# Optimization experiments

Measured on AMD Instinct MI355X. Metric: run time of the kernel, lower is better.

The kernel has to match this reference:

```python
import jax, jax.numpy as jnp
import numpy as np

EMBED_DIM = 1024
N_HEADS = 16
HEAD_DIM = EMBED_DIM // N_HEADS


def setup_inputs() -> dict:
    key = jax.random.key(0)
    k_x, k_wqkv, k_bqkv, k_wo, k_bo = jax.random.split(key, 5)
    s = 1.0 / np.sqrt(EMBED_DIM)
    return {
        "x": jax.random.normal(k_x, (2, 2048, EMBED_DIM), dtype=jnp.float32),
        "w_qkv": jax.random.uniform(k_wqkv, (EMBED_DIM, 3 * EMBED_DIM), jnp.float32, -s, s),
        "b_qkv": jax.random.uniform(k_bqkv, (3 * EMBED_DIM,), jnp.float32, -s, s),
        "w_out": jax.random.uniform(k_wo, (EMBED_DIM, EMBED_DIM), jnp.float32, -s, s),
        "b_out": jax.random.uniform(k_bo, (EMBED_DIM,), jnp.float32, -s, s),
    }


def reference(x, w_qkv, b_qkv, w_out, b_out):
    B, T, C = x.shape
    qkv = x @ w_qkv + b_qkv                      # [B,T,3C]
    q, k, v = jnp.split(qkv, 3, axis=-1)
    # [B,T,C] -> [B,H,T,D]
    def heads(t):
        return t.reshape(B, T, N_HEADS, HEAD_DIM).transpose(0, 2, 1, 3)
    q, k, v = heads(q), heads(k), heads(v)
    scale = 1.0 / np.sqrt(HEAD_DIM).astype(np.float32)
    scores = jnp.einsum("bhqd,bhkd->bhqk", q, k) * scale
    causal = jnp.tril(jnp.ones((T, T), dtype=bool))  # True where allowed
    scores = jnp.where(causal, scores, jnp.finfo(scores.dtype).min)
    attn = jax.nn.softmax(scores, axis=-1)
    out = jnp.einsum("bhqk,bhkd->bhqd", attn, v)
    out = out.transpose(0, 2, 1, 3).reshape(B, T, C)
    return out @ w_out + b_out
```

## Files before the change

### kernel.cpp

```cpp
#include <hip/hip_runtime.h>
#include <hip/hip_bf16.h>

typedef __attribute__((ext_vector_type(4))) float f32x4;
typedef __attribute__((ext_vector_type(8))) short bf16x8;

static __device__ __forceinline__ unsigned short f2bf(float f) {
  union { float f; unsigned u; } v;
  v.f = f;
  unsigned r = v.u + 0x7FFFu + ((v.u >> 16) & 1u);
  return (unsigned short)(r >> 16);
}

static __device__ __forceinline__ void gload16(const void* g, void* lds) {
  __builtin_amdgcn_global_load_lds(
      (const __attribute__((address_space(1))) unsigned int*)g,
      (__attribute__((address_space(3))) unsigned int*)lds, 16, 0, 0);
}

__global__ __launch_bounds__(256) void cast_bf16_kernel(
    const float* __restrict__ in, unsigned short* __restrict__ out) {
  int i = blockIdx.x * 256 + threadIdx.x;
  float4 v = reinterpret_cast<const float4*>(in)[i];
  ushort4 o;
  o.x = f2bf(v.x); o.y = f2bf(v.y); o.z = f2bf(v.z); o.w = f2bf(v.w);
  reinterpret_cast<ushort4*>(out)[i] = o;
}

__global__ __launch_bounds__(256) void transpose_cast_kernel(
    const float* __restrict__ in, unsigned short* __restrict__ out, int R, int C) {
  __shared__ float tile[32][33];
  int c0 = blockIdx.x * 32, r0 = blockIdx.y * 32;
  int tx = threadIdx.x & 31, ty = threadIdx.x >> 5;
#pragma unroll
  for (int i = 0; i < 32; i += 8)
    tile[ty + i][tx] = in[(size_t)(r0 + ty + i) * C + c0 + tx];
  __syncthreads();
#pragma unroll
  for (int i = 0; i < 32; i += 8)
    out[(size_t)(c0 + ty + i) * R + r0 + tx] = f2bf(tile[tx][ty + i]);
}

template <int MODE>
__global__ __launch_bounds__(256) void gemm_bf16(
    const unsigned short* __restrict__ A,
    const unsigned short* __restrict__ Bt,
    const float* __restrict__ bias,
    unsigned short* __restrict__ q_out,
    unsigned short* __restrict__ k_out,
    unsigned short* __restrict__ v_out,
    float* __restrict__ f_out) {
  __shared__ __align__(16) unsigned short As[128 * 32];
  __shared__ __align__(16) unsigned short Bs[128 * 32];

  const int tid = threadIdx.x;
  const int wid = tid >> 6, lane = tid & 63;
  const int l15 = lane & 15, g = lane >> 4;
  const int wm = wid >> 1, wn = wid & 1;
  const int n0 = blockIdx.x * 128, m0 = blockIdx.y * 128;

  f32x4 acc[4][4] = {};

  for (int k0 = 0; k0 < 1024; k0 += 32) {
    __syncthreads();
#pragma unroll
    for (int i = 0; i < 2; ++i) {
      int t = tid + i * 256;
      int row = t >> 2;
      int c8 = (t & 3) << 3;
      gload16(A + (size_t)(m0 + row) * 1024 + k0 + c8, As + (i * 256 + wid * 64) * 8);
      gload16(Bt + (size_t)(n0 + row) * 1024 + k0 + c8, Bs + (i * 256 + wid * 64) * 8);
    }
    __syncthreads();
    bf16x8 a[4], b[4];
#pragma unroll
    for (int mi = 0; mi < 4; ++mi)
      a[mi] = *reinterpret_cast<const bf16x8*>(As + (wm * 64 + mi * 16 + l15) * 32 + g * 8);
#pragma unroll
    for (int ni = 0; ni < 4; ++ni)
      b[ni] = *reinterpret_cast<const bf16x8*>(Bs + (wn * 64 + ni * 16 + l15) * 32 + g * 8);
#pragma unroll
    for (int mi = 0; mi < 4; ++mi)
#pragma unroll
      for (int ni = 0; ni < 4; ++ni)
        acc[mi][ni] = __builtin_amdgcn_mfma_f32_16x16x32_bf16(a[mi], b[ni], acc[mi][ni], 0, 0, 0);
  }

  if (MODE == 0) {
    const int which = n0 >> 10;
    unsigned short* dst = (which == 0) ? q_out : (which == 1) ? k_out : v_out;
#pragma unroll
    for (int ni = 0; ni < 4; ++ni) {
      int col = n0 + wn * 64 + ni * 16 + l15;
      int c = col & 1023;
      int h = c >> 6, d = c & 63;
      float bv = bias[col];
#pragma unroll
      for (int mi = 0; mi < 4; ++mi) {
#pragma unroll
        for (int r = 0; r < 4; ++r) {
          int rowg = m0 + wm * 64 + mi * 16 + g * 4 + r;
          int bb = rowg >> 11, tt = rowg & 2047;
          dst[((bb * 16 + h) * 2048 + tt) * 64 + d] = f2bf(acc[mi][ni][r] + bv);
        }
      }
    }
  } else {
#pragma unroll
    for (int ni = 0; ni < 4; ++ni) {
      int col = n0 + wn * 64 + ni * 16 + l15;
      float bv = bias[col];
#pragma unroll
      for (int mi = 0; mi < 4; ++mi)
#pragma unroll
        for (int r = 0; r < 4; ++r) {
          int rowg = m0 + wm * 64 + mi * 16 + g * 4 + r;
          f_out[(size_t)rowg * 1024 + col] = acc[mi][ni][r] + bv;
        }
    }
  }
}

#define KS_SZ (64 * 64)
#define VT_SZ (64 * 72)

__device__ __forceinline__ void attn_stage_K(const unsigned short* __restrict__ Kb,
                                             int k0, unsigned short* KsBuf,
                                             int tid, int wid) {
#pragma unroll
  for (int i = 0; i < 2; ++i) {
    int t = tid + i * 256;
    int row = t >> 3;
    int cb = (t & 7) << 4;
    int src = cb ^ ((row & 7) << 4);
    gload16((const char*)Kb + (size_t)(k0 + row) * 128 + src,
            (char*)KsBuf + (i * 256 + wid * 64) * 16);
  }
}

__device__ __forceinline__ void write_vt(unsigned short* VtBuf, int kvL, int d8,
                                         bf16x8 va, bf16x8 vb) {
#pragma unroll
  for (int j = 0; j < 8; ++j) {
    unsigned pk = (unsigned)(unsigned short)va[j] |
                  ((unsigned)(unsigned short)vb[j] << 16);
    *reinterpret_cast<unsigned*>(&VtBuf[(d8 + j) * 72 + kvL]) = pk;
  }
}

__device__ __forceinline__ void attn_run_qtile(
    const unsigned short* __restrict__ Qb,
    const unsigned short* __restrict__ Kb,
    const unsigned short* __restrict__ Vb,
    unsigned short* __restrict__ O,
    int b, int h, int q0, int nt,
    unsigned short* Ks, unsigned short* Vt, unsigned short* Ps,
    int tid, int wid, int l15, int g) {
  const float SC = 0.125f * 1.44269504f;

  bf16x8 qf[2];
  {
    const unsigned short* qrow = Qb + (size_t)(q0 + wid * 16 + l15) * 64;
    qf[0] = *reinterpret_cast<const bf16x8*>(qrow + g * 8);
    qf[1] = *reinterpret_cast<const bf16x8*>(qrow + 32 + g * 8);
  }

  float m_run = -1e30f, l_run = 0.0f;
  f32x4 ot[4] = {};
  const int qg = q0 + wid * 16 + l15;
  const int kvL = (tid & 31) * 2, d8 = (tid >> 5) * 8;

  attn_stage_K(Kb, 0, Ks, tid, wid);
  {
    const unsigned short* vp = Vb + (size_t)kvL * 64 + d8;
    bf16x8 va = *reinterpret_cast<const bf16x8*>(vp);
    bf16x8 vb = *reinterpret_cast<const bf16x8*>(vp + 64);
    write_vt(Vt, kvL, d8, va, vb);
  }
  __syncthreads();

  for (int t = 0; t < nt; ++t) {
    const unsigned short* KsC = Ks + (t & 1) * KS_SZ;
    const unsigned short* VtC = Vt + (t & 1) * VT_SZ;
    bf16x8 va, vb;
    const bool pf = (t + 1 < nt);
    if (pf) {
      attn_stage_K(Kb, (t + 1) << 6, Ks + ((t + 1) & 1) * KS_SZ, tid, wid);
      const unsigned short* vp = Vb + (size_t)(((t + 1) << 6) + kvL) * 64 + d8;
      va = *reinterpret_cast<const bf16x8*>(vp);
      vb = *reinterpret_cast<const bf16x8*>(vp + 64);
    }

    f32x4 s[4] = {};
    __builtin_amdgcn_s_setprio(1);
#pragma unroll
    for (int kk = 0; kk < 2; ++kk)
#pragma unroll
      for (int mi = 0; mi < 4; ++mi) {
        int row = mi * 16 + l15;
        int cb = (kk * 64 + g * 16) ^ ((row & 7) << 4);
        bf16x8 kf = *reinterpret_cast<const bf16x8*>((const char*)KsC + row * 128 + cb);
        s[mi] = __builtin_amdgcn_mfma_f32_16x16x32_bf16(kf, qf[kk], s[mi], 0, 0, 0);
      }
    __builtin_amdgcn_s_setprio(0);

    float tmax = -1e30f;
    if (t == nt - 1) {
      const int k0 = t << 6;
#pragma unroll
      for (int mi = 0; mi < 4; ++mi)
#pragma unroll
        for (int r = 0; r < 4; ++r) {
          int kvg = k0 + mi * 16 + g * 4 + r;
          float sv = s[mi][r] * SC;
          sv = (kvg <= qg) ? sv : -1e30f;
          s[mi][r] = sv;
          tmax = fmaxf(tmax, sv);
        }
    } else {
#pragma unroll
      for (int mi = 0; mi < 4; ++mi)
#pragma unroll
        for (int r = 0; r < 4; ++r) {
          float sv = s[mi][r] * SC;
          s[mi][r] = sv;
          tmax = fmaxf(tmax, sv);
        }
    }
    tmax = fmaxf(tmax, __shfl_xor(tmax, 16));
    tmax = fmaxf(tmax, __shfl_xor(tmax, 32));

    if (!__all(tmax <= m_run + 8.0f)) {
      float m_new = fmaxf(m_run, tmax);
      float corr = __builtin_amdgcn_exp2f(m_run - m_new);
      l_run *= corr;
#pragma unroll
      for (int mi = 0; mi < 4; ++mi)
#pragma unroll
        for (int r = 0; r < 4; ++r) ot[mi][r] *= corr;
      m_run = m_new;
    }

    float tsum = 0.f;
    const int qrow = wid * 16 + l15;
#pragma unroll
    for (int mi = 0; mi < 4; ++mi) {
#pragma unroll
      for (int r2 = 0; r2 < 2; ++r2) {
        float p0 = __builtin_amdgcn_exp2f(s[mi][2 * r2] - m_run);
        float p1 = __builtin_amdgcn_exp2f(s[mi][2 * r2 + 1] - m_run);
        tsum += p0 + p1;
        unsigned pk = (unsigned)f2bf(p0) | ((unsigned)f2bf(p1) << 16);
        *reinterpret_cast<unsigned*>(&Ps[qrow * 72 + mi * 16 + g * 4 + 2 * r2]) = pk;
      }
    }
    tsum += __shfl_xor(tsum, 16);
    tsum += __shfl_xor(tsum, 32);
    l_run += tsum;

    __builtin_amdgcn_s_setprio(1);
#pragma unroll
    for (int kk = 0; kk < 2; ++kk) {
      bf16x8 pfr = *reinterpret_cast<const bf16x8*>(Ps + qrow * 72 + kk * 32 + g * 8);
#pragma unroll
      for (int mi = 0; mi < 4; ++mi) {
        bf16x8 vf = *reinterpret_cast<const bf16x8*>(VtC + (mi * 16 + l15) * 72 + kk * 32 + g * 8);
        ot[mi] = __builtin_amdgcn_mfma_f32_16x16x32_bf16(vf, pfr, ot[mi], 0, 0, 0);
      }
    }
    __builtin_amdgcn_s_setprio(0);

    if (pf) write_vt(Vt + ((t + 1) & 1) * VT_SZ, kvL, d8, va, vb);
    __syncthreads();
  }

  float inv_l = 1.0f / l_run;
#pragma unroll
  for (int mi = 0; mi < 4; ++mi)
#pragma unroll
    for (int r = 0; r < 4; ++r) {
      int q = wid * 16 + l15;
      int d = mi * 16 + g * 4 + r;
      int cb = (d * 2) ^ ((q & 7) << 4);
      *reinterpret_cast<unsigned short*>((char*)Ks + q * 128 + cb) = f2bf(ot[mi][r] * inv_l);
    }
  __syncthreads();
#pragma unroll
  for (int i = 0; i < 2; ++i) {
    int t = tid + i * 256;
    int row = t >> 3;
    int cb = (t & 7) << 4;
    int sw = cb ^ ((row & 7) << 4);
    bf16x8 vv = *reinterpret_cast<const bf16x8*>((const char*)Ks + row * 128 + sw);
    *reinterpret_cast<bf16x8*>(O + ((size_t)(b * 2048 + q0 + row)) * 1024 + h * 64 + (cb >> 1)) = vv;
  }
  __syncthreads();
}

__global__ __launch_bounds__(256) void attn_fwd(
    const unsigned short* __restrict__ Q,
    const unsigned short* __restrict__ K,
    const unsigned short* __restrict__ V,
    unsigned short* __restrict__ O) {
  __shared__ __align__(16) unsigned short Ks[2 * KS_SZ];
  __shared__ __align__(16) unsigned short Vt[2 * VT_SZ];
  __shared__ __align__(16) unsigned short Ps[64 * 72];

  const int tid = threadIdx.x;
  const int wid = tid >> 6;
  const int l15 = tid & 15;
  const int g = (tid & 63) >> 4;

  int lin = blockIdx.x + (blockIdx.y << 4);
  int w = ((lin & 7) << 6) + (lin >> 3);
  const int pi = w & 15, bh = w >> 4;
  const int b = bh >> 4, h = bh & 15;

  const unsigned short* Qb = Q + (size_t)bh * 2048 * 64;
  const unsigned short* Kb = K + (size_t)bh * 2048 * 64;
  const unsigned short* Vb = V + (size_t)bh * 2048 * 64;

  attn_run_qtile(Qb, Kb, Vb, O, b, h, pi << 6, pi + 1, Ks, Vt, Ps, tid, wid, l15, g);
  attn_run_qtile(Qb, Kb, Vb, O, b, h, (31 - pi) << 6, 32 - pi, Ks, Vt, Ps, tid, wid, l15, g);
}

extern "C" void kernel_launch(void* const* d_in, const int* in_sizes, int n_in,
                              void* d_out, int out_size, void* d_ws, size_t ws_size,
                              hipStream_t stream) {
  const float* x = (const float*)d_in[0];
  const float* w_qkv = (const float*)d_in[1];
  const float* b_qkv = (const float*)d_in[2];
  const float* w_out = (const float*)d_in[3];
  const float* b_out = (const float*)d_in[4];
  float* out = (float*)d_out;
  char* ws = (char*)d_ws;

  unsigned short* xb    = (unsigned short*)d_out;
  unsigned short* wqkvT = (unsigned short*)(ws);
  unsigned short* woT   = (unsigned short*)(ws + 6291456);
  unsigned short* q_buf = (unsigned short*)(ws + 8388608);
  unsigned short* k_buf = (unsigned short*)(ws + 16777216);
  unsigned short* v_buf = (unsigned short*)(ws + 25165824);
  unsigned short* aout  = (unsigned short*)(ws + 33554432);

  cast_bf16_kernel<<<dim3(4096), dim3(256), 0, stream>>>(x, xb);
  transpose_cast_kernel<<<dim3(96, 32), dim3(256), 0, stream>>>(w_qkv, wqkvT, 1024, 3072);
  transpose_cast_kernel<<<dim3(32, 32), dim3(256), 0, stream>>>(w_out, woT, 1024, 1024);

  gemm_bf16<0><<<dim3(24, 32), dim3(256), 0, stream>>>(
      xb, wqkvT, b_qkv, q_buf, k_buf, v_buf, nullptr);

  attn_fwd<<<dim3(16, 32), dim3(256), 0, stream>>>(q_buf, k_buf, v_buf, aout);

  gemm_bf16<1><<<dim3(8, 32), dim3(256), 0, stream>>>(
      aout, woT, b_out, nullptr, nullptr, nullptr, out);
}
```

Measured before the change: 123.8 us.

## Fuse prep kernels, double-buffer GEMM LDS, shrink output GEMM tile

Merges the x cast and both weight transpose-casts into one launch, which removes two kernel launches. The GEMM gains double-buffered LDS so the next K-slice is loaded while MFMAs run on the current one, and the MFMA block is raised in priority. The output projection now uses BN=64 tiles, doubling its grid to 512 blocks to fill more CUs. The attention kernel only gets minor index hoisting. Costs are larger LDS use per block and a possible race: there is a single barrier per iteration while the async global-to-LDS loads are issued before the reads of the current buffer.

```diff
diff --git a/kernel.cpp b/kernel.cpp
--- a/kernel.cpp
+++ b/kernel.cpp
@@ -17,30 +17,41 @@
       (__attribute__((address_space(3))) unsigned int*)lds, 16, 0, 0);
 }
 
-__global__ __launch_bounds__(256) void cast_bf16_kernel(
-    const float* __restrict__ in, unsigned short* __restrict__ out) {
-  int i = blockIdx.x * 256 + threadIdx.x;
-  float4 v = reinterpret_cast<const float4*>(in)[i];
-  ushort4 o;
-  o.x = f2bf(v.x); o.y = f2bf(v.y); o.z = f2bf(v.z); o.w = f2bf(v.w);
-  reinterpret_cast<ushort4*>(out)[i] = o;
-}
-
-__global__ __launch_bounds__(256) void transpose_cast_kernel(
-    const float* __restrict__ in, unsigned short* __restrict__ out, int R, int C) {
+__global__ __launch_bounds__(256) void prep_kernel(
+    const float* __restrict__ x, const float* __restrict__ w_qkv,
+    const float* __restrict__ w_out, unsigned short* __restrict__ xb,
+    unsigned short* __restrict__ wqkvT, unsigned short* __restrict__ woT) {
   __shared__ float tile[32][33];
-  int c0 = blockIdx.x * 32, r0 = blockIdx.y * 32;
-  int tx = threadIdx.x & 31, ty = threadIdx.x >> 5;
+  const int bid = blockIdx.x, tid = threadIdx.x;
+  if (bid < 4096) {
+    int i = bid * 256 + tid;
+    float4 v = reinterpret_cast<const float4*>(x)[i];
+    ushort4 o;
+    o.x = f2bf(v.x); o.y = f2bf(v.y); o.z = f2bf(v.z); o.w = f2bf(v.w);
+    reinterpret_cast<ushort4*>(xb)[i] = o;
+    return;
+  }
+  const float* src; unsigned short* dst; int c0, r0, C;
+  if (bid < 7168) {
+    int t = bid - 4096;
+    src = w_qkv; dst = wqkvT; C = 3072;
+    c0 = (t % 96) * 32; r0 = (t / 96) * 32;
+  } else {
+    int t = bid - 7168;
+    src = w_out; dst = woT; C = 1024;
+    c0 = (t & 31) * 32; r0 = (t >> 5) * 32;
+  }
+  int tx = tid & 31, ty = tid >> 5;
 #pragma unroll
   for (int i = 0; i < 32; i += 8)
-    tile[ty + i][tx] = in[(size_t)(r0 + ty + i) * C + c0 + tx];
+    tile[ty + i][tx] = src[(size_t)(r0 + ty + i) * C + c0 + tx];
   __syncthreads();
 #pragma unroll
   for (int i = 0; i < 32; i += 8)
-    out[(size_t)(c0 + ty + i) * R + r0 + tx] = f2bf(tile[tx][ty + i]);
-}
-
-template <int MODE>
+    dst[(size_t)(c0 + ty + i) * 1024 + r0 + tx] = f2bf(tile[tx][ty + i]);
+}
+
+template <int MODE, int BN>
 __global__ __launch_bounds__(256) void gemm_bf16(
     const unsigned short* __restrict__ A,
     const unsigned short* __restrict__ Bt,
@@ -49,48 +60,62 @@
     unsigned short* __restrict__ k_out,
     unsigned short* __restrict__ v_out,
     float* __restrict__ f_out) {
-  __shared__ __align__(16) unsigned short As[128 * 32];
-  __shared__ __align__(16) unsigned short Bs[128 * 32];
+  constexpr int NB2 = BN / 32;
+  constexpr int NBL = BN / 64;
+  __shared__ __align__(16) unsigned short As[2][128 * 32];
+  __shared__ __align__(16) unsigned short Bs[2][BN * 32];
 
   const int tid = threadIdx.x;
   const int wid = tid >> 6, lane = tid & 63;
   const int l15 = lane & 15, g = lane >> 4;
   const int wm = wid >> 1, wn = wid & 1;
-  const int n0 = blockIdx.x * 128, m0 = blockIdx.y * 128;
-
-  f32x4 acc[4][4] = {};
-
-  for (int k0 = 0; k0 < 1024; k0 += 32) {
-    __syncthreads();
+  const int n0 = blockIdx.x * BN, m0 = blockIdx.y * 128;
+
+  f32x4 acc[4][NB2] = {};
+
+  auto stage = [&](int k0, int bsel) {
 #pragma unroll
     for (int i = 0; i < 2; ++i) {
       int t = tid + i * 256;
-      int row = t >> 2;
-      int c8 = (t & 3) << 3;
-      gload16(A + (size_t)(m0 + row) * 1024 + k0 + c8, As + (i * 256 + wid * 64) * 8);
-      gload16(Bt + (size_t)(n0 + row) * 1024 + k0 + c8, Bs + (i * 256 + wid * 64) * 8);
-    }
+      int row = t >> 2, c8 = (t & 3) << 3;
+      gload16(A + (size_t)(m0 + row) * 1024 + k0 + c8, &As[bsel][(i * 256 + wid * 64) * 8]);
+    }
+#pragma unroll
+    for (int i = 0; i < NBL; ++i) {
+      int t = tid + i * 256;
+      int row = t >> 2, c8 = (t & 3) << 3;
+      gload16(Bt + (size_t)(n0 + row) * 1024 + k0 + c8, &Bs[bsel][(i * 256 + wid * 64) * 8]);
+    }
+  };
+
+  stage(0, 0);
+  __syncthreads();
+  for (int ks = 0; ks < 32; ++ks) {
+    const int cur = ks & 1;
+    if (ks + 1 < 32) stage((ks + 1) * 32, cur ^ 1);
+    bf16x8 a[4], b[NB2];
+#pragma unroll
+    for (int mi = 0; mi < 4; ++mi)
+      a[mi] = *reinterpret_cast<const bf16x8*>(&As[cur][(wm * 64 + mi * 16 + l15) * 32 + g * 8]);
+#pragma unroll
+    for (int ni = 0; ni < NB2; ++ni)
+      b[ni] = *reinterpret_cast<const bf16x8*>(&Bs[cur][(wn * (BN / 2) + ni * 16 + l15) * 32 + g * 8]);
+    __builtin_amdgcn_s_setprio(1);
+#pragma unroll
+    for (int mi = 0; mi < 4; ++mi)
+#pragma unroll
+      for (int ni = 0; ni < NB2; ++ni)
+        acc[mi][ni] = __builtin_amdgcn_mfma_f32_16x16x32_bf16(a[mi], b[ni], acc[mi][ni], 0, 0, 0);
+    __builtin_amdgcn_s_setprio(0);
     __syncthreads();
-    bf16x8 a[4], b[4];
-#pragma unroll
-    for (int mi = 0; mi < 4; ++mi)
-      a[mi] = *reinterpret_cast<const bf16x8*>(As + (wm * 64 + mi * 16 + l15) * 32 + g * 8);
-#pragma unroll
-    for (int ni = 0; ni < 4; ++ni)
-      b[ni] = *reinterpret_cast<const bf16x8*>(Bs + (wn * 64 + ni * 16 + l15) * 32 + g * 8);
-#pragma unroll
-    for (int mi = 0; mi < 4; ++mi)
-#pragma unroll
-      for (int ni = 0; ni < 4; ++ni)
-        acc[mi][ni] = __builtin_amdgcn_mfma_f32_16x16x32_bf16(a[mi], b[ni], acc[mi][ni], 0, 0, 0);
   }
 
   if (MODE == 0) {
     const int which = n0 >> 10;
     unsigned short* dst = (which == 0) ? q_out : (which == 1) ? k_out : v_out;
 #pragma unroll
-    for (int ni = 0; ni < 4; ++ni) {
-      int col = n0 + wn * 64 + ni * 16 + l15;
+    for (int ni = 0; ni < NB2; ++ni) {
+      int col = n0 + wn * (BN / 2) + ni * 16 + l15;
       int c = col & 1023;
       int h = c >> 6, d = c & 63;
       float bv = bias[col];
@@ -106,8 +131,8 @@
     }
   } else {
 #pragma unroll
-    for (int ni = 0; ni < 4; ++ni) {
-      int col = n0 + wn * 64 + ni * 16 + l15;
+    for (int ni = 0; ni < NB2; ++ni) {
+      int col = n0 + wn * (BN / 2) + ni * 16 + l15;
       float bv = bias[col];
 #pragma unroll
       for (int mi = 0; mi < 4; ++mi)
@@ -168,6 +193,7 @@
   f32x4 ot[4] = {};
   const int qg = q0 + wid * 16 + l15;
   const int kvL = (tid & 31) * 2, d8 = (tid >> 5) * 8;
+  const int qrow = wid * 16 + l15;
 
   attn_stage_K(Kb, 0, Ks, tid, wid);
   {
@@ -241,7 +267,6 @@
     }
 
     float tsum = 0.f;
-    const int qrow = wid * 16 + l15;
 #pragma unroll
     for (int mi = 0; mi < 4; ++mi) {
 #pragma unroll
@@ -278,10 +303,9 @@
   for (int mi = 0; mi < 4; ++mi)
 #pragma unroll
     for (int r = 0; r < 4; ++r) {
-      int q = wid * 16 + l15;
       int d = mi * 16 + g * 4 + r;
-      int cb = (d * 2) ^ ((q & 7) << 4);
-      *reinterpret_cast<unsigned short*>((char*)Ks + q * 128 + cb) = f2bf(ot[mi][r] * inv_l);
+      int cb = (d * 2) ^ ((qrow & 7) << 4);
+      *reinterpret_cast<unsigned short*>((char*)Ks + qrow * 128 + cb) = f2bf(ot[mi][r] * inv_l);
     }
   __syncthreads();
 #pragma unroll
@@ -342,15 +366,13 @@
   unsigned short* v_buf = (unsigned short*)(ws + 25165824);
   unsigned short* aout  = (unsigned short*)(ws + 33554432);
 
-  cast_bf16_kernel<<<dim3(4096), dim3(256), 0, stream>>>(x, xb);
-  transpose_cast_kernel<<<dim3(96, 32), dim3(256), 0, stream>>>(w_qkv, wqkvT, 1024, 3072);
-  transpose_cast_kernel<<<dim3(32, 32), dim3(256), 0, stream>>>(w_out, woT, 1024, 1024);
-
-  gemm_bf16<0><<<dim3(24, 32), dim3(256), 0, stream>>>(
+  prep_kernel<<<dim3(8192), dim3(256), 0, stream>>>(x, w_qkv, w_out, xb, wqkvT, woT);
+
+  gemm_bf16<0, 128><<<dim3(24, 32), dim3(256), 0, stream>>>(
       xb, wqkvT, b_qkv, q_buf, k_buf, v_buf, nullptr);
 
   attn_fwd<<<dim3(16, 32), dim3(256), 0, stream>>>(q_buf, k_buf, v_buf, aout);
 
-  gemm_bf16<1><<<dim3(8, 32), dim3(256), 0, stream>>>(
+  gemm_bf16<1, 64><<<dim3(16, 32), dim3(256), 0, stream>>>(
       aout, woT, b_out, nullptr, nullptr, nullptr, out);
 }
```

After: 121.1 us. 2.2% less time.
